# Optimization experiments

Measured on AMD Instinct MI355X. Metric: run time of the kernel, lower is better.

## Reference

```python
import jax, jax.numpy as jnp
import numpy as np

BETA = 0.9
THRESHOLD = 1.0
SLOPE = 25.0  # snntorch fast_sigmoid default slope
T_STEPS = 64
IN_DIM, HID, NCLS = 256, 128, 8
BATCH = 16384


@jax.custom_vjp
def spike(u):
    # heaviside(u) with fast_sigmoid surrogate gradient
    return (u > 0).astype(u.dtype)

def _spike_fwd(u):
    return spike(u), u

def _spike_bwd(u, g):
    return (g / (SLOPE * jnp.abs(u) + 1.0) ** 2,)

spike.defvjp(_spike_fwd, _spike_bwd)


def setup_inputs() -> dict:
    key = jax.random.key(0)
    k1, k2, k3, k4, k5 = jax.random.split(key, 5)
    b1_bound = 1.0 / np.sqrt(IN_DIM)
    b2_bound = 1.0 / np.sqrt(HID)
    return {
        "x": jax.random.normal(k1, (BATCH, IN_DIM), jnp.float32),
        "W1": jax.random.uniform(k2, (HID, IN_DIM), jnp.float32, -b1_bound, b1_bound),
        "b1": jax.random.uniform(k3, (HID,), jnp.float32, -b1_bound, b1_bound),
        "W2": jax.random.uniform(k4, (NCLS, HID), jnp.float32, -b2_bound, b2_bound),
        "b2": jax.random.uniform(k5, (NCLS,), jnp.float32, -b2_bound, b2_bound),
    }


def reference(x, W1, b1, W2, b2):
    # fc1(x) is identical every timestep -> hoist out of the loop (same math)
    cur1 = x @ W1.T + b1  # [B, HID]

    def step(carry, _):
        mem1, mem2, acc = carry
        # snntorch Leaky (reset_mechanism='subtract'):
        # reset computed from incoming mem, detached
        reset1 = jax.lax.stop_gradient((mem1 - THRESHOLD > 0).astype(mem1.dtype))
        mem1 = BETA * mem1 + cur1 - reset1 * THRESHOLD
        spk1 = spike(mem1 - THRESHOLD)

        cur2 = spk1 @ W2.T + b2  # [B, NCLS]
        reset2 = jax.lax.stop_gradient((mem2 - THRESHOLD > 0).astype(mem2.dtype))
        mem2 = BETA * mem2 + cur2 - reset2 * THRESHOLD
        spk2 = spike(mem2 - THRESHOLD)
        return (mem1, mem2, acc + spk2), None

    mem1_0 = jnp.zeros((x.shape[0], HID), x.dtype)
    mem2_0 = jnp.zeros((x.shape[0], NCLS), x.dtype)
    acc0 = jnp.zeros((x.shape[0], NCLS), x.dtype)
    (_, _, out), _ = jax.lax.scan(step, (mem1_0, mem2_0, acc0), None, length=T_STEPS)
    return out
```

## Files before the change

kernel.cpp:

```cpp
#include <hip/hip_runtime.h>
#include <math.h>


#define T_STEPS 64
#define IN_DIM  256
#define HID     128
#define NCLS    8

#define A_THR  256
#define A_ROWS 32
#define A_KQ   16

__global__ __launch_bounds__(A_THR, 2)
void snn_gemm(const float* __restrict__ x, const float* __restrict__ W1,
              const float* __restrict__ b1, float* __restrict__ ws)
{
#pragma clang fp contract(off)
    __shared__ float4 w1c[A_KQ][HID + 2];
    __shared__ float  xcf[64 * 33];

    const int tid  = threadIdx.x;
    const int lane = tid & 63;
    const int wv   = __builtin_amdgcn_readfirstlane(tid >> 6);
    const size_t rowg0 = (size_t)blockIdx.x * A_ROWS;

    float accL[8], accH[8];
    #pragma unroll
    for (int j = 0; j < 8; ++j) { accL[j] = 0.0f; accH[j] = 0.0f; }

    #pragma unroll 1
    for (int ch = 0; ch < 4; ++ch) {
        const int kbase = ch * (A_KQ * 4);
        #pragma unroll
        for (int s = 0; s < 8; ++s) {
            const int idx = tid + s * A_THR;
            const int h = idx >> 4, kq = idx & 15;
            w1c[kq][h] = *(const float4*)(W1 + (size_t)h * IN_DIM + kbase + kq * 4);
        }
        #pragma unroll
        for (int s = 0; s < 2; ++s) {
            const int idx = tid + s * A_THR;
            const int rr = idx >> 4, kq = idx & 15;
            const float4 v = *(const float4*)(x + (rowg0 + rr) * IN_DIM + kbase + kq * 4);
            xcf[(4 * kq + 0) * 33 + rr] = v.x;
            xcf[(4 * kq + 1) * 33 + rr] = v.y;
            xcf[(4 * kq + 2) * 33 + rr] = v.z;
            xcf[(4 * kq + 3) * 33 + rr] = v.w;
        }
        __syncthreads();

        #pragma unroll 4
        for (int kq = 0; kq < A_KQ; ++kq) {
            const float4 wL = w1c[kq][lane];
            const float4 wH = w1c[kq][64 + lane];
            #pragma unroll
            for (int j = 0; j < 8; ++j) {
                const int rb = wv * 8 + j;
                const float x0 = xcf[(4 * kq + 0) * 33 + rb];
                const float x1 = xcf[(4 * kq + 1) * 33 + rb];
                const float x2 = xcf[(4 * kq + 2) * 33 + rb];
                const float x3 = xcf[(4 * kq + 3) * 33 + rb];
                float aL = accL[j], aH = accH[j];
                aL = fmaf(x0, wL.x, aL);
                aL = fmaf(x1, wL.y, aL);
                aL = fmaf(x2, wL.z, aL);
                aL = fmaf(x3, wL.w, aL);
                aH = fmaf(x0, wH.x, aH);
                aH = fmaf(x1, wH.y, aH);
                aH = fmaf(x2, wH.z, aH);
                aH = fmaf(x3, wH.w, aH);
                accL[j] = aL; accH[j] = aH;
            }
        }
        __syncthreads();
    }

    const float bL = b1[lane], bH = b1[64 + lane];
    #pragma unroll
    for (int j = 0; j < 8; ++j) {
        const size_t rg = rowg0 + wv * 8 + j;
        ws[rg * HID + lane]      = accL[j] + bL;
        ws[rg * HID + 64 + lane] = accH[j] + bH;
    }
}

#define B_RPB  32
#define B_THR  256
#define RSTR   260

static __device__ __forceinline__ unsigned int pkspk(float a, float b) {
    auto h = __builtin_amdgcn_cvt_pkrtz(a, b);
    return __builtin_bit_cast(unsigned int, h);
}

__global__ __launch_bounds__(B_THR, 2)
void snn_tloop(const float* __restrict__ ws, const float* __restrict__ W2,
               const float* __restrict__ b2, float* __restrict__ out)
{
#pragma clang fp contract(off)
    __shared__ unsigned int pk[B_RPB * RSTR];
    __shared__ float4 w2l[NCLS * 32];

    const int tid = threadIdx.x;
    const int r   = tid >> 3;
    const int q   = tid & 7;

    w2l[tid] = ((const float4*)W2)[tid];

    float cur1[16];
    {
        const float* src = ws + ((size_t)blockIdx.x * B_RPB + r) * HID + q * 16;
        #pragma unroll
        for (int i = 0; i < 4; ++i) {
            const float4 v = *(const float4*)(src + 4 * i);
            cur1[4*i+0] = v.x; cur1[4*i+1] = v.y;
            cur1[4*i+2] = v.z; cur1[4*i+3] = v.w;
        }
    }

    const int lane = tid & 63;
    const int brow = lane & 31;
    const int bcls = 2 * (tid >> 6) + (lane >> 5);
    const float b2c = b2[bcls];
    const float4* __restrict__ w2p = &w2l[bcls * 32];

    float mem1[16], spk1[16];
    #pragma unroll
    for (int i = 0; i < 16; ++i) { mem1[i] = 0.0f; spk1[i] = 0.0f; }
    float m2 = 0.0f, r2v = 0.0f, o = 0.0f;

    #pragma unroll 1
    for (int ts = 0; ts < T_STEPS; ts += 4) {
        #pragma unroll
        for (int j = 0; j < 4; ++j) {
            #pragma unroll
            for (int i = 0; i < 16; ++i) {
                float tmp = 0.9f * mem1[i];
                tmp = tmp + cur1[i];
                float m = tmp - spk1[i];
                mem1[i] = m;
                spk1[i] = (m > 1.0f) ? 1.0f : 0.0f;
            }
            unsigned int* dst = &pk[r * RSTR + j * 64 + q * 8];
            #pragma unroll
            for (int s = 0; s < 2; ++s) {
                uint4 pv;
                pv.x = pkspk(spk1[8*s+0], spk1[8*s+1]);
                pv.y = pkspk(spk1[8*s+2], spk1[8*s+3]);
                pv.z = pkspk(spk1[8*s+4], spk1[8*s+5]);
                pv.w = pkspk(spk1[8*s+6], spk1[8*s+7]);
                *(uint4*)(dst + 4 * s) = pv;
            }
        }
        __syncthreads();

        float a0 = 0.0f, a1 = 0.0f, a2 = 0.0f, a3 = 0.0f;
        const unsigned int* src = &pk[brow * RSTR];
#define FMIX_LO(A, P, W) \
        asm("v_fma_mix_f32 %0, %1, %2, %0 op_sel_hi:[1,0,0]" \
            : "+v"(A) : "v"(P), "v"(W));
#define FMIX_HI(A, P, W) \
        asm("v_fma_mix_f32 %0, %1, %2, %0 op_sel:[1,0,0] op_sel_hi:[1,0,0]" \
            : "+v"(A) : "v"(P), "v"(W));
#define TR(A, P) \
        FMIX_LO(A, P.x, wA.x) FMIX_HI(A, P.x, wA.y) \
        FMIX_LO(A, P.y, wA.z) FMIX_HI(A, P.y, wA.w) \
        FMIX_LO(A, P.z, wB.x) FMIX_HI(A, P.z, wB.y) \
        FMIX_LO(A, P.w, wB.z) FMIX_HI(A, P.w, wB.w)
        #pragma unroll
        for (int gg = 0; gg < 16; ++gg) {
            const float4 wA = w2p[2 * gg];
            const float4 wB = w2p[2 * gg + 1];
            const uint4 p0 = *(const uint4*)(src + 0 * 64 + 4 * gg);
            const uint4 p1 = *(const uint4*)(src + 1 * 64 + 4 * gg);
            const uint4 p2 = *(const uint4*)(src + 2 * 64 + 4 * gg);
            const uint4 p3 = *(const uint4*)(src + 3 * 64 + 4 * gg);
            TR(a0, p0) TR(a1, p1) TR(a2, p2) TR(a3, p3)
        }
#undef TR
#undef FMIX_HI
#undef FMIX_LO
        __syncthreads();

        const float aa[4] = {a0, a1, a2, a3};
        #pragma unroll
        for (int j = 0; j < 4; ++j) {
            const float c2 = aa[j] + b2c;
            float t2 = 0.9f * m2; t2 = t2 + c2; m2 = t2 - r2v;
            r2v = (m2 > 1.0f) ? 1.0f : 0.0f;
            o = o + r2v;
        }
    }

    out[((size_t)blockIdx.x * B_RPB + brow) * NCLS + bcls] = o;
}

extern "C" void kernel_launch(void* const* d_in, const int* in_sizes, int n_in,
                              void* d_out, int out_size, void* d_ws, size_t ws_size,
                              hipStream_t stream) {
    const float* x  = (const float*)d_in[0];
    const float* W1 = (const float*)d_in[1];
    const float* b1 = (const float*)d_in[2];
    const float* W2 = (const float*)d_in[3];
    const float* b2 = (const float*)d_in[4];
    float* out = (float*)d_out;
    float* cur_ws = (float*)d_ws;

    const int batch = in_sizes[0] / IN_DIM;
    snn_gemm<<<batch / A_ROWS, A_THR, 0, stream>>>(x, W1, b1, cur_ws);
    snn_tloop<<<batch / B_RPB, B_THR, 0, stream>>>(cur_ws, W2, b2, out);
}
```

Before: 149.0 us.

## Fuse fc1 GEMM and time-loop kernels, keep cur1 in shared memory

Merges the fc1 GEMM kernel and the spiking time-loop kernel into a single kernel. The per-block cur1 tile now stays in LDS instead of making a round trip through a global workspace, and one kernel launch disappears. LDS is aliased between the GEMM staging buffers, cur1, the spike buffer and W2, giving about 41 KB per block. That footprint may limit occupancy compared with the separate kernels, and the two phases no longer overlap across blocks the same way.

```diff
diff --git a/kernel.cpp b/kernel.cpp
--- a/kernel.cpp
+++ b/kernel.cpp
@@ -7,85 +7,9 @@
 #define HID     128
 #define NCLS    8
 
-#define A_THR  256
-#define A_ROWS 32
+#define ROWS   32
+#define THR    256
 #define A_KQ   16
-
-__global__ __launch_bounds__(A_THR, 2)
-void snn_gemm(const float* __restrict__ x, const float* __restrict__ W1,
-              const float* __restrict__ b1, float* __restrict__ ws)
-{
-#pragma clang fp contract(off)
-    __shared__ float4 w1c[A_KQ][HID + 2];
-    __shared__ float  xcf[64 * 33];
-
-    const int tid  = threadIdx.x;
-    const int lane = tid & 63;
-    const int wv   = __builtin_amdgcn_readfirstlane(tid >> 6);
-    const size_t rowg0 = (size_t)blockIdx.x * A_ROWS;
-
-    float accL[8], accH[8];
-    #pragma unroll
-    for (int j = 0; j < 8; ++j) { accL[j] = 0.0f; accH[j] = 0.0f; }
-
-    #pragma unroll 1
-    for (int ch = 0; ch < 4; ++ch) {
-        const int kbase = ch * (A_KQ * 4);
-        #pragma unroll
-        for (int s = 0; s < 8; ++s) {
-            const int idx = tid + s * A_THR;
-            const int h = idx >> 4, kq = idx & 15;
-            w1c[kq][h] = *(const float4*)(W1 + (size_t)h * IN_DIM + kbase + kq * 4);
-        }
-        #pragma unroll
-        for (int s = 0; s < 2; ++s) {
-            const int idx = tid + s * A_THR;
-            const int rr = idx >> 4, kq = idx & 15;
-            const float4 v = *(const float4*)(x + (rowg0 + rr) * IN_DIM + kbase + kq * 4);
-            xcf[(4 * kq + 0) * 33 + rr] = v.x;
-            xcf[(4 * kq + 1) * 33 + rr] = v.y;
-            xcf[(4 * kq + 2) * 33 + rr] = v.z;
-            xcf[(4 * kq + 3) * 33 + rr] = v.w;
-        }
-        __syncthreads();
-
-        #pragma unroll 4
-        for (int kq = 0; kq < A_KQ; ++kq) {
-            const float4 wL = w1c[kq][lane];
-            const float4 wH = w1c[kq][64 + lane];
-            #pragma unroll
-            for (int j = 0; j < 8; ++j) {
-                const int rb = wv * 8 + j;
-                const float x0 = xcf[(4 * kq + 0) * 33 + rb];
-                const float x1 = xcf[(4 * kq + 1) * 33 + rb];
-                const float x2 = xcf[(4 * kq + 2) * 33 + rb];
-                const float x3 = xcf[(4 * kq + 3) * 33 + rb];
-                float aL = accL[j], aH = accH[j];
-                aL = fmaf(x0, wL.x, aL);
-                aL = fmaf(x1, wL.y, aL);
-                aL = fmaf(x2, wL.z, aL);
-                aL = fmaf(x3, wL.w, aL);
-                aH = fmaf(x0, wH.x, aH);
-                aH = fmaf(x1, wH.y, aH);
-                aH = fmaf(x2, wH.z, aH);
-                aH = fmaf(x3, wH.w, aH);
-                accL[j] = aL; accH[j] = aH;
-            }
-        }
-        __syncthreads();
-    }
-
-    const float bL = b1[lane], bH = b1[64 + lane];
-    #pragma unroll
-    for (int j = 0; j < 8; ++j) {
-        const size_t rg = rowg0 + wv * 8 + j;
-        ws[rg * HID + lane]      = accL[j] + bL;
-        ws[rg * HID + 64 + lane] = accH[j] + bH;
-    }
-}
-
-#define B_RPB  32
-#define B_THR  256
 #define RSTR   260
 
 static __device__ __forceinline__ unsigned int pkspk(float a, float b) {
@@ -93,23 +17,94 @@
     return __builtin_bit_cast(unsigned int, h);
 }
 
-__global__ __launch_bounds__(B_THR, 2)
-void snn_tloop(const float* __restrict__ ws, const float* __restrict__ W2,
+__global__ __launch_bounds__(THR, 2)
+void snn_fused(const float* __restrict__ x, const float* __restrict__ W1,
+               const float* __restrict__ b1, const float* __restrict__ W2,
                const float* __restrict__ b2, float* __restrict__ out)
 {
 #pragma clang fp contract(off)
-    __shared__ unsigned int pk[B_RPB * RSTR];
-    __shared__ float4 w2l[NCLS * 32];
-
-    const int tid = threadIdx.x;
-    const int r   = tid >> 3;
-    const int q   = tid & 7;
-
-    w2l[tid] = ((const float4*)W2)[tid];
+    __shared__ __align__(16) char smem[41728];
+    float4 (* const w1c)[HID + 2] = (float4 (*)[HID + 2])smem;
+    float*        const xcf = (float*)(smem + 33280);
+    unsigned int* const pk  = (unsigned int*)smem;
+    float4*       const w2l = (float4*)(smem + 33280);
+    float*        const wsl = (float*)smem;
+
+    const int tid  = threadIdx.x;
+    const int lane = tid & 63;
+
+    {
+        const int wv = __builtin_amdgcn_readfirstlane(tid >> 6);
+        const size_t rowg0 = (size_t)blockIdx.x * ROWS;
+
+        float accL[8], accH[8];
+        #pragma unroll
+        for (int j = 0; j < 8; ++j) { accL[j] = 0.0f; accH[j] = 0.0f; }
+
+        #pragma unroll 1
+        for (int ch = 0; ch < 4; ++ch) {
+            const int kbase = ch * (A_KQ * 4);
+            #pragma unroll
+            for (int s = 0; s < 8; ++s) {
+                const int idx = tid + s * THR;
+                const int h = idx >> 4, kq = idx & 15;
+                w1c[kq][h] = *(const float4*)(W1 + (size_t)h * IN_DIM + kbase + kq * 4);
+            }
+            #pragma unroll
+            for (int s = 0; s < 2; ++s) {
+                const int idx = tid + s * THR;
+                const int rr = idx >> 4, kq = idx & 15;
+                const float4 v = *(const float4*)(x + (rowg0 + rr) * IN_DIM + kbase + kq * 4);
+                xcf[(4 * kq + 0) * 33 + rr] = v.x;
+                xcf[(4 * kq + 1) * 33 + rr] = v.y;
+                xcf[(4 * kq + 2) * 33 + rr] = v.z;
+                xcf[(4 * kq + 3) * 33 + rr] = v.w;
+            }
+            __syncthreads();
+
+            #pragma unroll 4
+            for (int kq = 0; kq < A_KQ; ++kq) {
+                const float4 wL = w1c[kq][lane];
+                const float4 wH = w1c[kq][64 + lane];
+                #pragma unroll
+                for (int j = 0; j < 8; ++j) {
+                    const int rb = wv * 8 + j;
+                    const float x0 = xcf[(4 * kq + 0) * 33 + rb];
+                    const float x1 = xcf[(4 * kq + 1) * 33 + rb];
+                    const float x2 = xcf[(4 * kq + 2) * 33 + rb];
+                    const float x3 = xcf[(4 * kq + 3) * 33 + rb];
+                    float aL = accL[j], aH = accH[j];
+                    aL = fmaf(x0, wL.x, aL);
+                    aL = fmaf(x1, wL.y, aL);
+                    aL = fmaf(x2, wL.z, aL);
+                    aL = fmaf(x3, wL.w, aL);
+                    aH = fmaf(x0, wH.x, aH);
+                    aH = fmaf(x1, wH.y, aH);
+                    aH = fmaf(x2, wH.z, aH);
+                    aH = fmaf(x3, wH.w, aH);
+                    accL[j] = aL; accH[j] = aH;
+                }
+            }
+            __syncthreads();
+        }
+
+        const float bL = b1[lane], bH = b1[64 + lane];
+        #pragma unroll
+        for (int j = 0; j < 8; ++j) {
+            const int rr = wv * 8 + j;
+            wsl[rr * HID + lane]      = accL[j] + bL;
+            wsl[rr * HID + 64 + lane] = accH[j] + bH;
+        }
+        w2l[tid] = ((const float4*)W2)[tid];
+    }
+    __syncthreads();
+
+    const int r = tid >> 3;
+    const int q = tid & 7;
 
     float cur1[16];
     {
-        const float* src = ws + ((size_t)blockIdx.x * B_RPB + r) * HID + q * 16;
+        const float* src = wsl + r * HID + q * 16;
         #pragma unroll
         for (int i = 0; i < 4; ++i) {
             const float4 v = *(const float4*)(src + 4 * i);
@@ -117,8 +112,8 @@
             cur1[4*i+2] = v.z; cur1[4*i+3] = v.w;
         }
     }
-
-    const int lane = tid & 63;
+    __syncthreads();
+
     const int brow = lane & 31;
     const int bcls = 2 * (tid >> 6) + (lane >> 5);
     const float b2c = b2[bcls];
@@ -192,7 +187,7 @@
         }
     }
 
-    out[((size_t)blockIdx.x * B_RPB + brow) * NCLS + bcls] = o;
+    out[((size_t)blockIdx.x * ROWS + brow) * NCLS + bcls] = o;
 }
 
 extern "C" void kernel_launch(void* const* d_in, const int* in_sizes, int n_in,
@@ -204,9 +199,8 @@
     const float* W2 = (const float*)d_in[3];
     const float* b2 = (const float*)d_in[4];
     float* out = (float*)d_out;
-    float* cur_ws = (float*)d_ws;
+    (void)d_ws; (void)ws_size;
 
     const int batch = in_sizes[0] / IN_DIM;
-    snn_gemm<<<batch / A_ROWS, A_THR, 0, stream>>>(x, W1, b1, cur_ws);
-    snn_tloop<<<batch / B_RPB, B_THR, 0, stream>>>(cur_ws, W2, b2, out);
+    snn_fused<<<batch / ROWS, THR, 0, stream>>>(x, W1, b1, W2, b2, out);
 }
```

Result: faster. 145.0 us (-2.7%).
